# Kernel optimization log

Measured on AMD Instinct MI355X. Metric: run time of the kernel, lower is better.

## Reference

```python
import jax, jax.numpy as jnp
import numpy as np

DIM = 256
NUM_HEADS = 4
HEAD_DIM = DIM // NUM_HEADS
WINDOW_SIZES = [2, 4, 8, 16]
SCALE = HEAD_DIM ** -0.5


def setup_inputs() -> dict:
    key = jax.random.key(0)
    k1, k2, k3, k4 = jax.random.split(key, 4)
    B, C, H, W = 8, DIM, 128, 128
    x = jax.random.normal(k1, (B, C, H, W), dtype=jnp.float32)
    # 1x1 conv weights stored as [out, in]
    qkv_w = jax.random.normal(k2, (3 * DIM, DIM), dtype=jnp.float32) * (DIM ** -0.5)
    proj_w = jax.random.normal(k3, (DIM, DIM), dtype=jnp.float32) * (DIM ** -0.5)
    proj_b = jax.random.normal(k4, (DIM,), dtype=jnp.float32) * 0.01
    return {"x": x, "qkv_w": qkv_w, "proj_w": proj_w, "proj_b": proj_b}


def _window_attn(q, k, v, ws):
    # q,k,v: [B, H, W, hd] for one head; windowed self-attention of size ws
    B, H, W, hd = q.shape
    hg, wg = H // ws, W // ws

    def part(t):
        # [B,H,W,hd] -> [B, hg*wg, ws*ws, hd]
        t = t.reshape(B, hg, ws, wg, ws, hd).transpose(0, 1, 3, 2, 4, 5)
        return t.reshape(B, hg * wg, ws * ws, hd)

    qw, kw, vw = part(q), part(k), part(v)
    attn = jnp.einsum('bgqd,bgkd->bgqk', qw, kw) * SCALE
    attn = jax.nn.softmax(attn, axis=-1)
    out = jnp.einsum('bgqk,bgkd->bgqd', attn, vw)
    # reassemble: [B, hg, wg, ws, ws, hd] -> [B, H, W, hd]
    out = out.reshape(B, hg, wg, ws, ws, hd).transpose(0, 1, 3, 2, 4, 5)
    return out.reshape(B, H, W, hd)


def reference(x, qkv_w, proj_w, proj_b):
    B, C, H, W = x.shape
    # 1x1 conv qkv: [B, 3*dim, H, W] -> [3, B, nh, H, W, hd]
    qkv = jnp.einsum('bchw,oc->bohw', x, qkv_w)
    qkv = qkv.reshape(B, 3, NUM_HEADS, HEAD_DIM, H, W).transpose(1, 0, 2, 4, 5, 3)
    q, k, v = qkv[0], qkv[1], qkv[2]
    outs = []
    for i, ws in enumerate(WINDOW_SIZES):
        outs.append(_window_attn(q[:, i], k[:, i], v[:, i], ws))
    y = jnp.concatenate(outs, axis=-1)  # [B, H, W, dim]
    y = jnp.einsum('bhwc,oc->bhwo', y, proj_w) + proj_b
    y = y.transpose(0, 3, 1, 2)  # [B, dim, H, W]
    return y + x
```

## Files before the change

### kernel.cpp

```cpp
#include <hip/hip_runtime.h>
#include <hip/hip_bf16.h>
#include <cstddef>
#include <cstdint>

typedef unsigned short u16;
typedef unsigned int uint32;
typedef __attribute__((ext_vector_type(8))) short bf16x8;
typedef __attribute__((ext_vector_type(4))) float f32x4;

#define SPATIAL 16384
#define TOTAL_M 131072

__device__ __forceinline__ u16 f2b(float f) {
  __hip_bfloat16 h = __float2bfloat16(f);
  return *reinterpret_cast<u16*>(&h);
}
__device__ __forceinline__ uint32 pk2(float a, float b) {
  return (uint32)f2b(a) | ((uint32)f2b(b) << 16);
}
__device__ __forceinline__ float blo(uint32 u) {
  union { uint32 u; float f; } c; c.u = u << 16; return c.f;
}
__device__ __forceinline__ float bhi(uint32 u) {
  union { uint32 u; float f; } c; c.u = u & 0xffff0000u; return c.f;
}

__device__ __forceinline__ void gload_lds16(const u16* g, u16* l) {
  __builtin_amdgcn_global_load_lds(
      (const __attribute__((address_space(1))) void*)g,
      (__attribute__((address_space(3))) void*)l, 16, 0, 0);
}

template <int WS>
__device__ __forceinline__ size_t tok_base(int gw, int tt) {
  constexpr int WG = 128 / WS;
  constexpr int NWIN = WG * WG;
  int bb = gw / NWIN, rr = gw % NWIN;
  int gy = rr / WG, gx = rr % WG;
  int yy = gy * WS + tt / WS, xx = gx * WS + tt % WS;
  return (((size_t)bb * 128 + yy) * 128 + xx) * 768;
}

__global__ __launch_bounds__(256) void prep(const float* __restrict__ x,
                                            const float* __restrict__ qw,
                                            const float* __restrict__ pw,
                                            u16* __restrict__ xT,
                                            u16* __restrict__ wq,
                                            u16* __restrict__ wp) {
  const int tid = threadIdx.x;
  const int bid = blockIdx.x;
  if (bid >= 2048) {
    const int t = (bid - 2048) * 256 + tid;
#pragma unroll
    for (int i = 0; i < 16; ++i) {
      const int e = i * 4096 + t;
      if (e < 49152) {
        float4 v = *(const float4*)&qw[(size_t)e * 4];
        ushort4 o;
        o.x = f2b(v.x); o.y = f2b(v.y); o.z = f2b(v.z); o.w = f2b(v.w);
        *(ushort4*)&wq[(size_t)e * 4] = o;
      } else {
        float4 v = *(const float4*)&pw[(size_t)(e - 49152) * 4];
        ushort4 o;
        o.x = f2b(v.x); o.y = f2b(v.y); o.z = f2b(v.z); o.w = f2b(v.w);
        *(ushort4*)&wp[(size_t)(e - 49152) * 4] = o;
      }
    }
    return;
  }
  __shared__ u16 Ts[64 * 256];
  const int b = bid >> 8;
  const int sp0 = (bid & 255) * 64;
#pragma unroll
  for (int it = 0; it < 16; ++it) {
    int e = it * 256 + tid;
    int k = e >> 4;
    int c4 = (e & 15) * 4;
    float4 v = *(const float4*)&x[(((size_t)(b * 256 + k)) << 14) + sp0 + c4];
    Ts[(c4 + 0) * 256 + (k ^ ((((c4 + 0)) & 31) << 3))] = f2b(v.x);
    Ts[(c4 + 1) * 256 + (k ^ ((((c4 + 1)) & 31) << 3))] = f2b(v.y);
    Ts[(c4 + 2) * 256 + (k ^ ((((c4 + 2)) & 31) << 3))] = f2b(v.z);
    Ts[(c4 + 3) * 256 + (k ^ ((((c4 + 3)) & 31) << 3))] = f2b(v.w);
  }
  __syncthreads();
#pragma unroll
  for (int it = 0; it < 8; ++it) {
    int e = it * 256 + tid;
    int sp = e >> 5;
    int kc = (e & 31) * 8;
    bf16x8 row = *(const bf16x8*)&Ts[sp * 256 + (kc ^ ((sp & 31) << 3))];
    *(bf16x8*)&xT[((size_t)(b * 16384 + sp0 + sp)) * 256 + kc] = row;
  }
}

__global__ __launch_bounds__(256) void gemm_qkv(const u16* __restrict__ xT,
                                                const u16* __restrict__ wq,
                                                u16* __restrict__ qkv) {
  __shared__ u16 As[128 * 64];
  __shared__ u16 Bs[128 * 64];
  const int tid = threadIdx.x;
  const int n0 = blockIdx.x * 128;
  const int m0 = blockIdx.y * 128;
  const int lane = tid & 63, w = tid >> 6;
  const int wr = w >> 1, wc = w & 1;
  const int fr = lane & 15, fk = lane >> 4;
  const int frx = (fr & 7) << 3;
  f32x4 acc[4][4] = {};
  for (int kt = 0; kt < 4; ++kt) {
    const int k0 = kt * 64;
#pragma unroll
    for (int it = 0; it < 4; ++it) {
      int e = it * 256 + tid;
      int row = e >> 3;
      int kcs = ((e & 7) * 8) ^ ((row & 7) << 3);
      u16* la = &As[(it * 256 + (tid & 192)) * 8];
      u16* lb = &Bs[(it * 256 + (tid & 192)) * 8];
      gload_lds16(&xT[((size_t)(m0 + row) << 8) + k0 + kcs], la);
      gload_lds16(&wq[((size_t)(n0 + row) << 8) + k0 + kcs], lb);
    }
    __syncthreads();
#pragma unroll
    for (int kk = 0; kk < 2; ++kk) {
      const int kb = (kk * 32 + fk * 8) ^ frx;
      bf16x8 af[4], bfr[4];
#pragma unroll
      for (int i = 0; i < 4; ++i) {
        af[i] = *(const bf16x8*)&As[(wr * 64 + i * 16 + fr) * 64 + kb];
        bfr[i] = *(const bf16x8*)&Bs[(wc * 64 + i * 16 + fr) * 64 + kb];
      }
#pragma unroll
      for (int i = 0; i < 4; ++i)
#pragma unroll
        for (int j = 0; j < 4; ++j)
          acc[i][j] = __builtin_amdgcn_mfma_f32_16x16x32_bf16(bfr[j], af[i], acc[i][j], 0, 0, 0);
    }
    __syncthreads();
  }
#pragma unroll
  for (int i = 0; i < 4; ++i) {
    const size_t row = (size_t)(m0 + wr * 64 + i * 16 + fr) * 768;
#pragma unroll
    for (int j = 0; j < 4; ++j) {
      uint2 p;
      p.x = pk2(acc[i][j][0], acc[i][j][1]);
      p.y = pk2(acc[i][j][2], acc[i][j][3]);
      *(uint2*)&qkv[row + n0 + wc * 64 + j * 16 + fk * 4] = p;
    }
  }
}

template <int WS, int NT>
__device__ __forceinline__ void win_attn_body(u16* __restrict__ qkv, int head,
                                              int bid, u16* __restrict__ smem) {
  constexpr int T = WS * WS;
  constexpr int G = NT / T;
  u16 (*Ks)[72] = (u16(*)[72])smem;
  u16 (*Vs)[72] = (u16(*)[72])(smem + NT * 72);
  const int tid = threadIdx.x;
  const int gw0 = bid * G;
  const int qoff = head * 64;

#pragma unroll
  for (int i = 0; i < 8; ++i) {
    int e8 = i * NT + tid;
    int tok = e8 >> 3;
    int d8 = (e8 & 7) * 8;
    size_t base = tok_base<WS>(gw0 + tok / T, tok % T);
    *(bf16x8*)&Ks[tok][d8] = *(const bf16x8*)&qkv[base + 256 + qoff + d8];
    *(bf16x8*)&Vs[tok][d8] = *(const bf16x8*)&qkv[base + 512 + qoff + d8];
  }
  __syncthreads();

  const int myw = tid / T;
  const int mytt = tid % T;
  const size_t mybase = tok_base<WS>(gw0 + myw, mytt);

  float q[64];
#pragma unroll
  for (int d8i = 0; d8i < 8; ++d8i) {
    union { bf16x8 v; uint32 u[4]; } U;
    U.v = *(const bf16x8*)&qkv[mybase + qoff + d8i * 8];
    q[d8i * 8 + 0] = blo(U.u[0]); q[d8i * 8 + 1] = bhi(U.u[0]);
    q[d8i * 8 + 2] = blo(U.u[1]); q[d8i * 8 + 3] = bhi(U.u[1]);
    q[d8i * 8 + 4] = blo(U.u[2]); q[d8i * 8 + 5] = bhi(U.u[2]);
    q[d8i * 8 + 6] = blo(U.u[3]); q[d8i * 8 + 7] = bhi(U.u[3]);
  }
  const int rbase = myw * T;

  float sarr[T];
  float mmax = -1e30f;
#pragma unroll
  for (int j = 0; j < T; ++j) {
    float s = 0.f;
#pragma unroll
    for (int d4 = 0; d4 < 16; ++d4) {
      uint2 k2 = *(const uint2*)&Ks[rbase + j][d4 * 4];
      s = fmaf(q[d4 * 4 + 0], blo(k2.x), s);
      s = fmaf(q[d4 * 4 + 1], bhi(k2.x), s);
      s = fmaf(q[d4 * 4 + 2], blo(k2.y), s);
      s = fmaf(q[d4 * 4 + 3], bhi(k2.y), s);
    }
    sarr[j] = s * 0.125f;
    mmax = fmaxf(mmax, sarr[j]);
  }
  float lsum = 0.f;
#pragma unroll
  for (int j = 0; j < T; ++j) {
    sarr[j] = __expf(sarr[j] - mmax);
    lsum += sarr[j];
  }
  const float inv = 1.f / lsum;

  float acc[64] = {};
#pragma unroll
  for (int j = 0; j < T; ++j) {
    const float p = sarr[j] * inv;
#pragma unroll
    for (int d4 = 0; d4 < 16; ++d4) {
      uint2 v2 = *(const uint2*)&Vs[rbase + j][d4 * 4];
      acc[d4 * 4 + 0] = fmaf(p, blo(v2.x), acc[d4 * 4 + 0]);
      acc[d4 * 4 + 1] = fmaf(p, bhi(v2.x), acc[d4 * 4 + 1]);
      acc[d4 * 4 + 2] = fmaf(p, blo(v2.y), acc[d4 * 4 + 2]);
      acc[d4 * 4 + 3] = fmaf(p, bhi(v2.y), acc[d4 * 4 + 3]);
    }
  }
#pragma unroll
  for (int d8i = 0; d8i < 8; ++d8i) {
    union { bf16x8 v; uint32 u[4]; } U;
    U.u[0] = pk2(acc[d8i * 8 + 0], acc[d8i * 8 + 1]);
    U.u[1] = pk2(acc[d8i * 8 + 2], acc[d8i * 8 + 3]);
    U.u[2] = pk2(acc[d8i * 8 + 4], acc[d8i * 8 + 5]);
    U.u[3] = pk2(acc[d8i * 8 + 6], acc[d8i * 8 + 7]);
    *(bf16x8*)&qkv[mybase + qoff + d8i * 8] = U.v;
  }
}

template <int WS, int NW, int G>
__device__ __forceinline__ void win_mfma_body(u16* __restrict__ qkv, int head,
                                              int bid, u16* __restrict__ smem) {
  constexpr int T = WS * WS;
  constexpr int TOK = G * T;
  constexpr int KT = T / 16;
  constexpr int KS = T / 32;
  constexpr int PL = T + 8;
  constexpr int VP = TOK + 8;
  constexpr int NT = NW * 64;
  constexpr int QPW = (G * T / 16) / NW;
  u16* Ks = smem;
  u16* Vt = smem + TOK * 72;
  u16* Plds = Vt + 64 * VP;
  const int tid = threadIdx.x;
  const int gw0 = bid * G;
  const int qoff = head * 64;

#pragma unroll
  for (int it = 0; it < TOK * 8 / NT; ++it) {
    int e8 = it * NT + tid;
    int tok = e8 >> 3;
    int d8 = (e8 & 7) * 8;
    int win = tok / T, tt = tok % T;
    size_t base = tok_base<WS>(gw0 + win, tt);
    union { bf16x8 v; uint32 u[4]; } KK, VV;
    KK.v = *(const bf16x8*)&qkv[base + 256 + qoff + d8];
    VV.v = *(const bf16x8*)&qkv[base + 512 + qoff + d8];
    *(bf16x8*)&Ks[tok * 72 + d8] = KK.v;
#pragma unroll
    for (int z = 0; z < 4; ++z) {
      Vt[(d8 + 2 * z + 0) * VP + tok] = (u16)(VV.u[z] & 0xffffu);
      Vt[(d8 + 2 * z + 1) * VP + tok] = (u16)(VV.u[z] >> 16);
    }
  }
  __syncthreads();

  const int w = tid >> 6, lane = tid & 63;
  const int fr = lane & 15, fk = lane >> 4;
  u16* prow = &Plds[(w * 16 + fr) * PL];

  for (int qi = 0; qi < QPW; ++qi) {
    const int qg = w * QPW + qi;
    const int win = qg / (T / 16);
    const int qt = qg % (T / 16);
    const int gw = gw0 + win;

    const size_t qb = tok_base<WS>(gw, qt * 16 + fr) + qoff;
    bf16x8 qf[2];
#pragma unroll
    for (int ds = 0; ds < 2; ++ds)
      qf[ds] = *(const bf16x8*)&qkv[qb + ds * 32 + fk * 8];

    f32x4 sv[KT];
#pragma unroll
    for (int kt = 0; kt < KT; ++kt) {
      const u16* krow = &Ks[(win * T + kt * 16 + fr) * 72];
      bf16x8 k0 = *(const bf16x8*)&krow[fk * 8];
      bf16x8 k1 = *(const bf16x8*)&krow[32 + fk * 8];
      f32x4 s = {};
      s = __builtin_amdgcn_mfma_f32_16x16x32_bf16(k0, qf[0], s, 0, 0, 0);
      s = __builtin_amdgcn_mfma_f32_16x16x32_bf16(k1, qf[1], s, 0, 0, 0);
      sv[kt] = s;
    }

    float rmax = -3e38f;
#pragma unroll
    for (int kt = 0; kt < KT; ++kt)
#pragma unroll
      for (int r = 0; r < 4; ++r) rmax = fmaxf(rmax, sv[kt][r]);
    rmax = fmaxf(rmax, __shfl_xor(rmax, 16));
    rmax = fmaxf(rmax, __shfl_xor(rmax, 32));
    const float m = rmax * 0.125f;
    float l = 0.f;
#pragma unroll
    for (int kt = 0; kt < KT; ++kt)
#pragma unroll
      for (int r = 0; r < 4; ++r) {
        float ev = __expf(sv[kt][r] * 0.125f - m);
        sv[kt][r] = ev;
        l += ev;
      }
    l += __shfl_xor(l, 16);
    l += __shfl_xor(l, 32);
    const float linv = 1.f / l;

#pragma unroll
    for (int kt = 0; kt < KT; ++kt) {
      uint2 pp;
      pp.x = pk2(sv[kt][0], sv[kt][1]);
      pp.y = pk2(sv[kt][2], sv[kt][3]);
      *(uint2*)&prow[kt * 16 + fk * 4] = pp;
    }
    __asm__ __volatile__("s_waitcnt lgkmcnt(0)" ::: "memory");
    __builtin_amdgcn_sched_barrier(0);

    f32x4 ov[4] = {};
#pragma unroll
    for (int ks = 0; ks < KS; ++ks) {
      bf16x8 pf = *(const bf16x8*)&prow[ks * 32 + fk * 8];
#pragma unroll
      for (int dt = 0; dt < 4; ++dt) {
        bf16x8 vf = *(const bf16x8*)&Vt[(dt * 16 + fr) * VP + win * T + ks * 32 + fk * 8];
        ov[dt] = __builtin_amdgcn_mfma_f32_16x16x32_bf16(pf, vf, ov[dt], 0, 0, 0);
      }
    }

#pragma unroll
    for (int r = 0; r < 4; ++r) {
      float lr = __shfl(linv, fk * 4 + r);
      size_t ob = tok_base<WS>(gw, qt * 16 + fk * 4 + r) + qoff;
#pragma unroll
      for (int dt = 0; dt < 4; ++dt)
        qkv[ob + dt * 16 + fr] = f2b(ov[dt][r] * lr);
    }
  }
}

__global__ __launch_bounds__(512) void attn_all(u16* __restrict__ qkv) {
  __shared__ u16 smem[79360];
  const int bid = blockIdx.x;
  if (bid < 512)
    win_mfma_body<16, 8, 1>(qkv, 3, bid, smem);
  else if (bid < 768)
    win_mfma_body<8, 8, 8>(qkv, 2, bid - 512, smem);
  else if (bid < 1024)
    win_attn_body<4, 512>(qkv, 1, bid - 768, smem);
  else
    win_attn_body<2, 512>(qkv, 0, bid - 1024, smem);
}

__global__ __launch_bounds__(256) void gemm_proj(const u16* __restrict__ qkv,
                                                 const u16* __restrict__ wp,
                                                 const float* __restrict__ bias,
                                                 const float* __restrict__ x,
                                                 float* __restrict__ out) {
  __shared__ u16 As[2][128 * 64];
  __shared__ u16 Bs[2][128 * 64];
  const int tid = threadIdx.x;
  const int bid = blockIdx.x;
  const int logical = (bid & 7) * 256 + (bid >> 3);
  const int m0 = (logical >> 1) * 128;
  const int n0 = (logical & 1) * 128;
  const int lane = tid & 63, w = tid >> 6;
  const int wr = w >> 1, wc = w & 1;
  const int fr = lane & 15, fk = lane >> 4;
  const int frx = (fr & 7) << 3;
  const int kcs = ((tid & 7) * 8) ^ (((tid >> 3) & 7) << 3);
  const int srow = tid >> 3;
  const int b = m0 >> 14;
  f32x4 acc[4][4] = {};

#define STAGE_PRJ(B, KT)                                                     \
  do {                                                                       \
    const int k0s = (KT)*64;                                                 \
    _Pragma("unroll") for (int it = 0; it < 4; ++it) {                       \
      int row = it * 32 + srow;                                              \
      u16* la = &As[B][(it * 256 + (tid & 192)) * 8];                        \
      u16* lb = &Bs[B][(it * 256 + (tid & 192)) * 8];                        \
      gload_lds16(&qkv[(size_t)(m0 + row) * 768 + k0s + kcs], la);           \
      gload_lds16(&wp[((size_t)(n0 + row) << 8) + k0s + kcs], lb);           \
    }                                                                        \
  } while (0)

#define COMP_PRJ(B)                                                          \
  do {                                                                       \
    _Pragma("unroll") for (int kk = 0; kk < 2; ++kk) {                       \
      const int kb = (kk * 32 + fk * 8) ^ frx;                               \
      bf16x8 af[4], bfr[4];                                                  \
      _Pragma("unroll") for (int i = 0; i < 4; ++i) {                        \
        af[i] = *(const bf16x8*)&As[B][(wr * 64 + i * 16 + fr) * 64 + kb];   \
        bfr[i] = *(const bf16x8*)&Bs[B][(wc * 64 + i * 16 + fr) * 64 + kb];  \
      }                                                                      \
      _Pragma("unroll") for (int i = 0; i < 4; ++i)                          \
          _Pragma("unroll") for (int j = 0; j < 4; ++j) acc[i][j] =          \
          __builtin_amdgcn_mfma_f32_16x16x32_bf16(af[i], bfr[j],             \
                                                  acc[i][j], 0, 0, 0);       \
    }                                                                        \
  } while (0)

#define PHASE(WAITN)                                                         \
  asm volatile("s_waitcnt vmcnt(" #WAITN ")" ::: "memory");                  \
  __builtin_amdgcn_s_barrier();                                              \
  __builtin_amdgcn_sched_barrier(0)

#define PHASE_END()                                                          \
  __builtin_amdgcn_sched_barrier(0);                                         \
  __builtin_amdgcn_s_barrier()

  STAGE_PRJ(0, 0);
  STAGE_PRJ(1, 1);
  PHASE(8);
  COMP_PRJ(0);
  PHASE_END();
  STAGE_PRJ(0, 2);
  PHASE(8);
  COMP_PRJ(1);
  PHASE_END();
  STAGE_PRJ(1, 3);
  PHASE(8);
  COMP_PRJ(0);
  PHASE_END();
  PHASE(0);
  COMP_PRJ(1);
#undef STAGE_PRJ
#undef COMP_PRJ
#undef PHASE
#undef PHASE_END

#pragma unroll
  for (int i = 0; i < 4; ++i) {
    const int sp = (m0 & 16383) + wr * 64 + i * 16 + fk * 4;
#pragma unroll
    for (int j = 0; j < 4; ++j) {
      const int n = n0 + wc * 64 + j * 16 + fr;
      const size_t o = ((size_t)(b * 256 + n) << 14) + sp;
      const float4 r4 = *(const float4*)&x[o];
      const float bb = bias[n];
      float4 v = make_float4(acc[i][j][0] + bb + r4.x, acc[i][j][1] + bb + r4.y,
                             acc[i][j][2] + bb + r4.z, acc[i][j][3] + bb + r4.w);
      *(float4*)&out[o] = v;
    }
  }
}

extern "C" void kernel_launch(void* const* d_in, const int* in_sizes, int n_in,
                              void* d_out, int out_size, void* d_ws, size_t ws_size,
                              hipStream_t stream) {
  const float* x = (const float*)d_in[0];
  const float* qkv_w = (const float*)d_in[1];
  const float* proj_w = (const float*)d_in[2];
  const float* proj_b = (const float*)d_in[3];
  float* out = (float*)d_out;
  u16* qkv = (u16*)d_ws;
  u16* xT = qkv + (size_t)131072 * 768;
  u16* wq = xT + (size_t)131072 * 256;
  u16* wp = wq + (size_t)768 * 256;

  prep<<<2064, 256, 0, stream>>>(x, qkv_w, proj_w, xT, wq, wp);
  gemm_qkv<<<dim3(6, 1024), 256, 0, stream>>>(xT, wq, qkv);
  attn_all<<<1280, 512, 0, stream>>>(qkv);
  gemm_proj<<<2048, 256, 0, stream>>>(qkv, wp, proj_b, x, out);
}
```

Baseline: 292.8 us.

## Double-buffer QKV GEMM with 32-wide K stages and async load pipelining

Replaces the single-buffered 64-wide K loop in the QKV projection GEMM with a double-buffered pipeline of 32-wide K tiles. Each tile's global-to-LDS loads are issued before computing on the other buffer, using explicit vmcnt waits and raw barriers in place of two __syncthreads per iteration. The LDS swizzle is reworked for the 32-column row layout. The aim is to hide global load latency behind MFMA work; it uses more barrier phases, each with less compute to cover the latency.

```diff
diff --git a/kernel.cpp b/kernel.cpp
--- a/kernel.cpp
+++ b/kernel.cpp
@@ -96,46 +96,69 @@
 __global__ __launch_bounds__(256) void gemm_qkv(const u16* __restrict__ xT,
                                                 const u16* __restrict__ wq,
                                                 u16* __restrict__ qkv) {
-  __shared__ u16 As[128 * 64];
-  __shared__ u16 Bs[128 * 64];
+  __shared__ u16 As[2][128 * 32];
+  __shared__ u16 Bs[2][128 * 32];
   const int tid = threadIdx.x;
   const int n0 = blockIdx.x * 128;
   const int m0 = blockIdx.y * 128;
   const int lane = tid & 63, w = tid >> 6;
   const int wr = w >> 1, wc = w & 1;
   const int fr = lane & 15, fk = lane >> 4;
-  const int frx = (fr & 7) << 3;
+  const int kxor = (fr & 3) << 3;
+  const int kcs = ((tid & 3) * 8) ^ (((tid >> 2) & 3) << 3);
   f32x4 acc[4][4] = {};
-  for (int kt = 0; kt < 4; ++kt) {
-    const int k0 = kt * 64;
-#pragma unroll
-    for (int it = 0; it < 4; ++it) {
-      int e = it * 256 + tid;
-      int row = e >> 3;
-      int kcs = ((e & 7) * 8) ^ ((row & 7) << 3);
-      u16* la = &As[(it * 256 + (tid & 192)) * 8];
-      u16* lb = &Bs[(it * 256 + (tid & 192)) * 8];
-      gload_lds16(&xT[((size_t)(m0 + row) << 8) + k0 + kcs], la);
-      gload_lds16(&wq[((size_t)(n0 + row) << 8) + k0 + kcs], lb);
-    }
-    __syncthreads();
-#pragma unroll
-    for (int kk = 0; kk < 2; ++kk) {
-      const int kb = (kk * 32 + fk * 8) ^ frx;
-      bf16x8 af[4], bfr[4];
-#pragma unroll
-      for (int i = 0; i < 4; ++i) {
-        af[i] = *(const bf16x8*)&As[(wr * 64 + i * 16 + fr) * 64 + kb];
-        bfr[i] = *(const bf16x8*)&Bs[(wc * 64 + i * 16 + fr) * 64 + kb];
-      }
-#pragma unroll
-      for (int i = 0; i < 4; ++i)
-#pragma unroll
-        for (int j = 0; j < 4; ++j)
-          acc[i][j] = __builtin_amdgcn_mfma_f32_16x16x32_bf16(bfr[j], af[i], acc[i][j], 0, 0, 0);
-    }
-    __syncthreads();
-  }
+
+#define STAGE_Q(B, KT)                                                       \
+  do {                                                                       \
+    const int k0s = (KT)*32;                                                 \
+    _Pragma("unroll") for (int it = 0; it < 2; ++it) {                       \
+      int row = it * 64 + (tid >> 2);                                        \
+      u16* la = &As[B][(it * 256 + (tid & 192)) * 8];                        \
+      u16* lb = &Bs[B][(it * 256 + (tid & 192)) * 8];                        \
+      gload_lds16(&xT[((size_t)(m0 + row) << 8) + k0s + kcs], la);           \
+      gload_lds16(&wq[((size_t)(n0 + row) << 8) + k0s + kcs], lb);           \
+    }                                                                        \
+  } while (0)
+
+#define COMP_Q(B)                                                            \
+  do {                                                                       \
+    bf16x8 af[4], bfr[4];                                                    \
+    _Pragma("unroll") for (int i = 0; i < 4; ++i) {                          \
+      af[i] = *(const bf16x8*)&As[B][(wr * 64 + i * 16 + fr) * 32 +          \
+                                     ((fk << 3) ^ kxor)];                    \
+      bfr[i] = *(const bf16x8*)&Bs[B][(wc * 64 + i * 16 + fr) * 32 +         \
+                                      ((fk << 3) ^ kxor)];                   \
+    }                                                                        \
+    _Pragma("unroll") for (int i = 0; i < 4; ++i)                            \
+        _Pragma("unroll") for (int j = 0; j < 4; ++j) acc[i][j] =            \
+        __builtin_amdgcn_mfma_f32_16x16x32_bf16(bfr[j], af[i],               \
+                                                acc[i][j], 0, 0, 0);         \
+  } while (0)
+
+#define PHASE_Q(WAITN)                                                       \
+  asm volatile("s_waitcnt vmcnt(" #WAITN ")" ::: "memory");                  \
+  __builtin_amdgcn_s_barrier();                                              \
+  __builtin_amdgcn_sched_barrier(0)
+
+#define PHASE_QEND()                                                         \
+  __builtin_amdgcn_sched_barrier(0);                                         \
+  __builtin_amdgcn_s_barrier()
+
+  STAGE_Q(0, 0);
+  STAGE_Q(1, 1);
+  PHASE_Q(4); COMP_Q(0); PHASE_QEND(); STAGE_Q(0, 2);
+  PHASE_Q(4); COMP_Q(1); PHASE_QEND(); STAGE_Q(1, 3);
+  PHASE_Q(4); COMP_Q(0); PHASE_QEND(); STAGE_Q(0, 4);
+  PHASE_Q(4); COMP_Q(1); PHASE_QEND(); STAGE_Q(1, 5);
+  PHASE_Q(4); COMP_Q(0); PHASE_QEND(); STAGE_Q(0, 6);
+  PHASE_Q(4); COMP_Q(1); PHASE_QEND(); STAGE_Q(1, 7);
+  PHASE_Q(4); COMP_Q(0); PHASE_QEND();
+  PHASE_Q(0); COMP_Q(1);
+#undef STAGE_Q
+#undef COMP_Q
+#undef PHASE_Q
+#undef PHASE_QEND
+
 #pragma unroll
   for (int i = 0; i < 4; ++i) {
     const size_t row = (size_t)(m0 + wr * 64 + i * 16 + fr) * 768;
@@ -420,7 +443,7 @@
   __builtin_amdgcn_s_barrier();                                              \
   __builtin_amdgcn_sched_barrier(0)
 
-#define PHASE_END()                                                          \
+#define PHASE_END()                                                         \
   __builtin_amdgcn_sched_barrier(0);                                         \
   __builtin_amdgcn_s_barrier()
 
```

Measured after the change: 302.9 us. +3.5%, slower.
